# Kernel optimization log

Hardware: AMD Instinct MI355X
Metric: run time of the kernel (lower is better)

Reference implementation:

```python
import jax, jax.numpy as jnp
import numpy as np

# Fully-refined octree (branching=2, initial_levels=7) == dense grid of resolution 128.
R = 128            # voxel grid resolution per axis (2**initial_levels)
SH_DIM = 9         # (sh_degree+1)**2, sh_degree=2
DATA_DIM = 28      # 3*SH_DIM + 1 (RGB SH coeffs + density)
N_STEPS = 128      # fixed ray-march step count (render_opt.n_steps)
BG = 1.0           # background brightness


def sh_basis(d):
    """Real SH basis up to degree 2 for unit directions d: [N,3] -> [N,9]."""
    x, y, z = d[:, 0], d[:, 1], d[:, 2]
    C0 = 0.28209479177387814
    C1 = 0.4886025119029199
    C2 = (1.0925484305920792, -1.0925484305920792, 0.31539156525252005,
          -1.0925484305920792, 0.5462742152960396)
    return jnp.stack([
        jnp.full_like(x, C0),
        -C1 * y, C1 * z, -C1 * x,
        C2[0] * x * y, C2[1] * y * z,
        C2[2] * (2.0 * z * z - x * x - y * y),
        C2[3] * x * z, C2[4] * (x * x - y * y),
    ], axis=-1)


def trilerp(grid, pts):
    """Trilinear interpolation. grid [R,R,R,C], pts [N,3] in grid coords."""
    Rg = grid.shape[0]
    p = jnp.clip(pts, 0.0, Rg - 1.0 - 1e-4)
    p0 = jnp.floor(p).astype(jnp.int32)
    w = p - p0.astype(p.dtype)
    out = jnp.zeros((pts.shape[0], grid.shape[-1]), grid.dtype)
    for dx in (0, 1):
        wx = w[:, 0] if dx else 1.0 - w[:, 0]
        for dy in (0, 1):
            wy = w[:, 1] if dy else 1.0 - w[:, 1]
            for dz in (0, 1):
                wz = w[:, 2] if dz else 1.0 - w[:, 2]
                out = out + (wx * wy * wz)[:, None] * grid[p0[:, 0] + dx, p0[:, 1] + dy, p0[:, 2] + dz]
    return out


def _render(grid, rays_o, rays_d, scaling, offset):
    dirs = rays_d / jnp.linalg.norm(rays_d, axis=-1, keepdims=True)   # world viewdirs
    o = rays_o * scaling + offset                                      # tree coords in [0,1]^3
    d = dirs * scaling
    delta_scale = 1.0 / jnp.linalg.norm(d, axis=-1)                    # world-space step scale
    invd = 1.0 / jnp.where(jnp.abs(d) > 1e-9, d, 1e-9)
    t1 = (0.0 - o) * invd
    t2 = (1.0 - o) * invd
    tmin = jnp.maximum(jnp.max(jnp.minimum(t1, t2), axis=-1), 0.0)
    tmax = jnp.min(jnp.maximum(t1, t2), axis=-1)
    valid = tmax > tmin
    dt = jnp.where(valid, (tmax - tmin) / N_STEPS, 0.0)                # per-ray step length
    basis = sh_basis(dirs)                                             # [N,9]
    N = rays_o.shape[0]

    def step(carry, i):
        T, rgb = carry
        t = tmin + (i.astype(grid.dtype) + 0.5) * dt
        pos = o + t[:, None] * d                                       # [N,3] in [0,1]^3
        vals = trilerp(grid, pos * R - 0.5)                            # [N,28]
        sigma = jnp.where(valid, jax.nn.relu(vals[:, -1]), 0.0)
        coeffs = vals[:, :3 * SH_DIM].reshape(N, 3, SH_DIM)
        c = jax.nn.sigmoid(jnp.einsum('nj,ncj->nc', basis, coeffs))    # [N,3]
        alpha = 1.0 - jnp.exp(-sigma * dt * delta_scale)
        rgb = rgb + (T * alpha)[:, None] * c
        T = T * (1.0 - alpha)
        return (T, rgb), None

    init = (jnp.ones((N,), grid.dtype), jnp.zeros((N, 3), grid.dtype))
    (T, rgb), _ = jax.lax.scan(step, init, jnp.arange(N_STEPS))
    return rgb + T[:, None] * BG


def setup_inputs() -> dict:
    key = jax.random.key(0)
    k1, k2, k3 = jax.random.split(key, 3)
    N = 32768
    rays_o = jax.random.uniform(k1, (N, 3), jnp.float32)               # inside unit cube
    rays_d = jax.random.normal(k2, (N, 3), jnp.float32)
    grid = jax.random.normal(k3, (R, R, R, DATA_DIM), jnp.float32) * 0.1  # octree leaf data
    scaling = jnp.ones((3,), jnp.float32)                              # 0.5/radius, radius=0.5
    offset = jnp.zeros((3,), jnp.float32)                              # 0.5 - center*scaling
    return {"rays_o": rays_o, "rays_d": rays_d, "grid": grid,
            "scaling": scaling, "offset": offset}


def reference(rays_o, rays_d, grid, scaling, offset):
    return _render(grid, rays_o, rays_d, scaling, offset)
```

## Files before the change

kernel.cpp:

```cpp
#include <hip/hip_runtime.h>
#include <math.h>

#define RGRID 128
#define NSTEPS 128
#define DATA_DIM 28

__device__ __forceinline__ float fast_rcp(float x) { return __builtin_amdgcn_rcpf(x); }

__global__ __launch_bounds__(256) void render_kernel(
    const float* __restrict__ rays_o,
    const float* __restrict__ rays_d,
    const float* __restrict__ grid,
    const float* __restrict__ scaling,
    const float* __restrict__ offset,
    float* __restrict__ out, int N)
{
    int tid = blockIdx.x * blockDim.x + threadIdx.x;
    int ray = tid >> 6;
    int lane = tid & 63;
    int s = lane >> 3;
    int c = lane & 7;
    if (ray >= N) return;

    float ox = rays_o[ray * 3 + 0], oy = rays_o[ray * 3 + 1], oz = rays_o[ray * 3 + 2];
    float rdx = rays_d[ray * 3 + 0], rdy = rays_d[ray * 3 + 1], rdz = rays_d[ray * 3 + 2];
    float sx = scaling[0], sy = scaling[1], sz = scaling[2];
    float fx = offset[0], fy = offset[1], fz = offset[2];

    float dn = rsqrtf(rdx * rdx + rdy * rdy + rdz * rdz);
    float dirx = rdx * dn, diry = rdy * dn, dirz = rdz * dn;

    float o0 = ox * sx + fx, o1 = oy * sy + fy, o2 = oz * sz + fz;
    float d0 = dirx * sx, d1 = diry * sy, d2 = dirz * sz;
    float delta_scale = rsqrtf(d0 * d0 + d1 * d1 + d2 * d2);

    float a0 = fabsf(d0) > 1e-9f ? d0 : 1e-9f;
    float a1 = fabsf(d1) > 1e-9f ? d1 : 1e-9f;
    float a2 = fabsf(d2) > 1e-9f ? d2 : 1e-9f;
    float i0 = 1.0f / a0, i1 = 1.0f / a1, i2 = 1.0f / a2;

    float t1x = (0.0f - o0) * i0, t2x = (1.0f - o0) * i0;
    float t1y = (0.0f - o1) * i1, t2y = (1.0f - o1) * i1;
    float t1z = (0.0f - o2) * i2, t2z = (1.0f - o2) * i2;
    float tmin = fmaxf(fmaxf(fminf(t1x, t2x), fminf(t1y, t2y)), fminf(t1z, t2z));
    tmin = fmaxf(tmin, 0.0f);
    float tmax = fminf(fminf(fmaxf(t1x, t2x), fmaxf(t1y, t2y)), fmaxf(t1z, t2z));
    bool valid = tmax > tmin;
    float dt = valid ? (tmax - tmin) * (1.0f / NSTEPS) : 0.0f;
    float sig_scale = dt * delta_scale;

    const float C0 = 0.28209479177387814f;
    const float C1 = 0.4886025119029199f;
    float b0 = C0;
    float b1 = -C1 * diry;
    float b2 = C1 * dirz;
    float b3 = -C1 * dirx;
    float b4 = 1.0925484305920792f * dirx * diry;
    float b5 = -1.0925484305920792f * diry * dirz;
    float b6 = 0.31539156525252005f * (2.0f * dirz * dirz - dirx * dirx - diry * diry);
    float b7 = -1.0925484305920792f * dirx * dirz;
    float b8 = 0.5462742152960396f * (dirx * dirx - diry * diry);

    int cdx = (c >> 2) & 1, cdy = (c >> 1) & 1, cdz = c & 1;
    int laneoff = (cdx << 14) + (cdy << 7) + cdz;
    float fsx = cdx ? 1.0f : -1.0f, fbx = cdx ? 0.0f : 1.0f;
    float fsy = cdy ? 1.0f : -1.0f, fby = cdy ? 0.0f : 1.0f;
    float fsz = cdz ? 1.0f : -1.0f, fbz = cdz ? 0.0f : 1.0f;

    float T = 1.0f, accr = 0.0f, accg = 0.0f, accb = 0.0f;
    float soff = (float)s + 0.5f;

    auto calc = [&](int base, const float4*& gp, float& wgt) {
        float t = tmin + ((float)base + soff) * dt;
        float px = o0 + t * d0, py = o1 + t * d1, pz = o2 + t * d2;
        float gx = fminf(fmaxf(px * (float)RGRID - 0.5f, 0.0f), 126.9999f);
        float gy = fminf(fmaxf(py * (float)RGRID - 0.5f, 0.0f), 126.9999f);
        float gz = fminf(fmaxf(pz * (float)RGRID - 0.5f, 0.0f), 126.9999f);
        float flx = floorf(gx), fly = floorf(gy), flz = floorf(gz);
        int ix = (int)flx, iy = (int)fly, iz = (int)flz;
        float wx = gx - flx, wy = gy - fly, wz = gz - flz;
        wgt = (fsx * wx + fbx) * (fsy * wy + fby) * (fsz * wz + fbz);
        int vox = (ix << 14) + (iy << 7) + iz + laneoff;
        gp = (const float4*)(grid + (size_t)vox * DATA_DIM);
    };

    auto compute = [&](float4 v0, float4 v1, float4 v2, float4 v3,
                       float4 v4, float4 v5, float4 v6, float wgt) {
        float vr = b0 * v0.x + b1 * v0.y + b2 * v0.z + b3 * v0.w
                 + b4 * v1.x + b5 * v1.y + b6 * v1.z + b7 * v1.w + b8 * v2.x;
        float vg = b0 * v2.y + b1 * v2.z + b2 * v2.w
                 + b3 * v3.x + b4 * v3.y + b5 * v3.z + b6 * v3.w
                 + b7 * v4.x + b8 * v4.y;
        float vb = b0 * v4.z + b1 * v4.w
                 + b2 * v5.x + b3 * v5.y + b4 * v5.z + b5 * v5.w
                 + b6 * v6.x + b7 * v6.y + b8 * v6.z;
        float vs = v6.w;

        vr *= wgt; vg *= wgt; vb *= wgt; vs *= wgt;

        #pragma unroll
        for (int m = 1; m < 8; m <<= 1) {
            vr += __shfl_xor(vr, m);
            vg += __shfl_xor(vg, m);
            vb += __shfl_xor(vb, m);
            vs += __shfl_xor(vs, m);
        }

        float sigma = valid ? fmaxf(vs, 0.0f) : 0.0f;
        float alpha = 1.0f - __expf(-sigma * sig_scale);
        float av = 1.0f - alpha;
        float br = alpha * fast_rcp(1.0f + __expf(-vr));
        float bg = alpha * fast_rcp(1.0f + __expf(-vg));
        float bb = alpha * fast_rcp(1.0f + __expf(-vb));

        #pragma unroll
        for (int d = 8; d < 64; d <<= 1) {
            float pa  = __shfl_up(av, d);
            float pbr = __shfl_up(br, d);
            float pbg = __shfl_up(bg, d);
            float pbb = __shfl_up(bb, d);
            if (lane >= d) {
                br = pbr + pa * br;
                bg = pbg + pa * bg;
                bb = pbb + pa * bb;
                av = pa * av;
            }
        }

        accr += T * br;
        accg += T * bg;
        accb += T * bb;
        T *= av;
    };

    const float4 *gpA, *gpB;
    float wA, wB;
    float4 A0, A1, A2, A3, A4, A5, A6;
    float4 B0, B1, B2, B3, B4, B5, B6;

    calc(0, gpA, wA);
    A0 = gpA[0]; A1 = gpA[1]; A2 = gpA[2]; A3 = gpA[3];
    A4 = gpA[4]; A5 = gpA[5]; A6 = gpA[6];

    for (int base = 0; base < NSTEPS - 16; base += 16) {
        calc(base + 8, gpB, wB);
        B0 = gpB[0]; B1 = gpB[1]; B2 = gpB[2]; B3 = gpB[3];
        B4 = gpB[4]; B5 = gpB[5]; B6 = gpB[6];
        compute(A0, A1, A2, A3, A4, A5, A6, wA);

        calc(base + 16, gpA, wA);
        A0 = gpA[0]; A1 = gpA[1]; A2 = gpA[2]; A3 = gpA[3];
        A4 = gpA[4]; A5 = gpA[5]; A6 = gpA[6];
        compute(B0, B1, B2, B3, B4, B5, B6, wB);
    }

    calc(NSTEPS - 8, gpB, wB);
    B0 = gpB[0]; B1 = gpB[1]; B2 = gpB[2]; B3 = gpB[3];
    B4 = gpB[4]; B5 = gpB[5]; B6 = gpB[6];
    compute(A0, A1, A2, A3, A4, A5, A6, wA);
    compute(B0, B1, B2, B3, B4, B5, B6, wB);

    if (lane == 63) {
        out[ray * 3 + 0] = accr + T * 1.0f;
        out[ray * 3 + 1] = accg + T * 1.0f;
        out[ray * 3 + 2] = accb + T * 1.0f;
    }
}

extern "C" void kernel_launch(void* const* d_in, const int* in_sizes, int n_in,
                              void* d_out, int out_size, void* d_ws, size_t ws_size,
                              hipStream_t stream) {
    const float* rays_o  = (const float*)d_in[0];
    const float* rays_d  = (const float*)d_in[1];
    const float* grid    = (const float*)d_in[2];
    const float* scaling = (const float*)d_in[3];
    const float* offset  = (const float*)d_in[4];
    float* out = (float*)d_out;
    int N = in_sizes[0] / 3;

    int threads = 256;
    long long total = (long long)N * 64;
    int blocks = (int)((total + threads - 1) / threads);
    render_kernel<<<blocks, threads, 0, stream>>>(rays_o, rays_d, grid, scaling, offset, out, N);
}
```

Before: 502.7 us.

## Repack voxel grid to packed fp16 and use dot2 for SH evaluation

Each call first runs a pre-pass that converts the fp32 grid into 64-byte packed fp16 records, laid out so each colour's SH coefficients line up with the packed basis pairs. The render kernel then gathers half as many bytes per trilinear corner and evaluates the SH dot products with fdot2 instructions. This targets the gather bandwidth and cache footprint of the ray march. In exchange it adds a full-grid read and write on every call and lowers the precision of the stored coefficients and basis values. The fallback fp32 path, used when the workspace is too small, drops software pipelining and writes its result from lane 0 instead of lane 63, which looks wrong for the scanned transmittance.

```diff
diff --git a/kernel.cpp b/kernel.cpp
--- a/kernel.cpp
+++ b/kernel.cpp
@@ -4,10 +4,232 @@
 #define RGRID 128
 #define NSTEPS 128
 #define DATA_DIM 28
+#define NVOX (RGRID * RGRID * RGRID)
+
+typedef _Float16 h2 __attribute__((ext_vector_type(2)));
 
 __device__ __forceinline__ float fast_rcp(float x) { return __builtin_amdgcn_rcpf(x); }
 
-__global__ __launch_bounds__(256) void render_kernel(
+__device__ __forceinline__ float dot2acc(h2 a, h2 b, float c) {
+#if __has_builtin(__builtin_amdgcn_fdot2)
+    return __builtin_amdgcn_fdot2(a, b, c, false);
+#else
+    return c + (float)a[0] * (float)b[0] + (float)a[1] * (float)b[1];
+#endif
+}
+
+__device__ __forceinline__ unsigned pk(float a, float b) {
+    h2 t;
+    t[0] = (_Float16)a;
+    t[1] = (_Float16)b;
+    return __builtin_bit_cast(unsigned, t);
+}
+
+__device__ __forceinline__ h2 bc(unsigned w) { return __builtin_bit_cast(h2, w); }
+
+__global__ __launch_bounds__(256) void repack_kernel(
+    const float* __restrict__ grid, unsigned* __restrict__ ws)
+{
+    int v = blockIdx.x * blockDim.x + threadIdx.x;
+    if (v >= NVOX) return;
+    const float4* src = (const float4*)(grid + (size_t)v * DATA_DIM);
+    float4 f0 = src[0], f1 = src[1], f2 = src[2], f3 = src[3];
+    float4 f4 = src[4], f5 = src[5], f6 = src[6];
+
+    uint4 o0, o1, o2;
+    uint2 o3;
+    o0.x = pk(f0.x, f0.y); o0.y = pk(f0.z, f0.w); o0.z = pk(f1.x, f1.y); o0.w = pk(f1.z, f1.w);
+    o1.x = pk(f2.y, f2.z); o1.y = pk(f2.w, f3.x); o1.z = pk(f3.y, f3.z); o1.w = pk(f3.w, f4.x);
+    o2.x = pk(f4.z, f4.w); o2.y = pk(f5.x, f5.y); o2.z = pk(f5.z, f5.w); o2.w = pk(f6.x, f6.y);
+    o3.x = pk(f2.x, f4.y);
+    o3.y = pk(f6.z, f6.w);
+
+    unsigned* dst = ws + ((size_t)v << 4);
+    *(uint4*)(dst + 0) = o0;
+    *(uint4*)(dst + 4) = o1;
+    *(uint4*)(dst + 8) = o2;
+    *(uint2*)(dst + 12) = o3;
+}
+
+__global__ __launch_bounds__(256) void render_fp16(
+    const float* __restrict__ rays_o,
+    const float* __restrict__ rays_d,
+    const unsigned* __restrict__ vox16,
+    const float* __restrict__ scaling,
+    const float* __restrict__ offset,
+    float* __restrict__ out, int N)
+{
+    int tid = blockIdx.x * blockDim.x + threadIdx.x;
+    int ray = tid >> 6;
+    int lane = tid & 63;
+    int s = lane >> 3;
+    int c = lane & 7;
+    if (ray >= N) return;
+
+    float ox = rays_o[ray * 3 + 0], oy = rays_o[ray * 3 + 1], oz = rays_o[ray * 3 + 2];
+    float rdx = rays_d[ray * 3 + 0], rdy = rays_d[ray * 3 + 1], rdz = rays_d[ray * 3 + 2];
+    float sx = scaling[0], sy = scaling[1], sz = scaling[2];
+    float fx = offset[0], fy = offset[1], fz = offset[2];
+
+    float dn = rsqrtf(rdx * rdx + rdy * rdy + rdz * rdz);
+    float dirx = rdx * dn, diry = rdy * dn, dirz = rdz * dn;
+
+    float o0 = ox * sx + fx, o1 = oy * sy + fy, o2 = oz * sz + fz;
+    float d0 = dirx * sx, d1 = diry * sy, d2 = dirz * sz;
+    float delta_scale = rsqrtf(d0 * d0 + d1 * d1 + d2 * d2);
+
+    float a0 = fabsf(d0) > 1e-9f ? d0 : 1e-9f;
+    float a1 = fabsf(d1) > 1e-9f ? d1 : 1e-9f;
+    float a2 = fabsf(d2) > 1e-9f ? d2 : 1e-9f;
+    float i0 = 1.0f / a0, i1 = 1.0f / a1, i2 = 1.0f / a2;
+
+    float t1x = (0.0f - o0) * i0, t2x = (1.0f - o0) * i0;
+    float t1y = (0.0f - o1) * i1, t2y = (1.0f - o1) * i1;
+    float t1z = (0.0f - o2) * i2, t2z = (1.0f - o2) * i2;
+    float tmin = fmaxf(fmaxf(fminf(t1x, t2x), fminf(t1y, t2y)), fminf(t1z, t2z));
+    tmin = fmaxf(tmin, 0.0f);
+    float tmax = fminf(fminf(fmaxf(t1x, t2x), fmaxf(t1y, t2y)), fmaxf(t1z, t2z));
+    bool valid = tmax > tmin;
+    float dt = valid ? (tmax - tmin) * (1.0f / NSTEPS) : 0.0f;
+    float sig_scale = dt * delta_scale;
+
+    const float C0 = 0.28209479177387814f;
+    const float C1 = 0.4886025119029199f;
+    float b0f = C0;
+    float b1f = -C1 * diry;
+    float b2f = C1 * dirz;
+    float b3f = -C1 * dirx;
+    float b4f = 1.0925484305920792f * dirx * diry;
+    float b5f = -1.0925484305920792f * diry * dirz;
+    float b6f = 0.31539156525252005f * (2.0f * dirz * dirz - dirx * dirx - diry * diry);
+    float b7f = -1.0925484305920792f * dirx * dirz;
+    float b8f = 0.5462742152960396f * (dirx * dirx - diry * diry);
+    h2 hb01, hb23, hb45, hb67;
+    hb01[0] = (_Float16)b0f; hb01[1] = (_Float16)b1f;
+    hb23[0] = (_Float16)b2f; hb23[1] = (_Float16)b3f;
+    hb45[0] = (_Float16)b4f; hb45[1] = (_Float16)b5f;
+    hb67[0] = (_Float16)b6f; hb67[1] = (_Float16)b7f;
+
+    int cdx = (c >> 2) & 1, cdy = (c >> 1) & 1, cdz = c & 1;
+    int laneoff = (cdx << 14) + (cdy << 7) + cdz;
+    float fsx = cdx ? 1.0f : -1.0f, fbx = cdx ? 0.0f : 1.0f;
+    float fsy = cdy ? 1.0f : -1.0f, fby = cdy ? 0.0f : 1.0f;
+    float fsz = cdz ? 1.0f : -1.0f, fbz = cdz ? 0.0f : 1.0f;
+
+    float T = 1.0f, accr = 0.0f, accg = 0.0f, accb = 0.0f;
+    float soff = (float)s + 0.5f;
+
+    auto calc = [&](int base, const unsigned*& gp, float& wgt) {
+        float t = tmin + ((float)base + soff) * dt;
+        float px = o0 + t * d0, py = o1 + t * d1, pz = o2 + t * d2;
+        float gx = fminf(fmaxf(px * (float)RGRID - 0.5f, 0.0f), 126.9999f);
+        float gy = fminf(fmaxf(py * (float)RGRID - 0.5f, 0.0f), 126.9999f);
+        float gz = fminf(fmaxf(pz * (float)RGRID - 0.5f, 0.0f), 126.9999f);
+        float flx = floorf(gx), fly = floorf(gy), flz = floorf(gz);
+        int ix = (int)flx, iy = (int)fly, iz = (int)flz;
+        float wx = gx - flx, wy = gy - fly, wz = gz - flz;
+        wgt = (fsx * wx + fbx) * (fsy * wy + fby) * (fsz * wz + fbz);
+        int vox = (ix << 14) + (iy << 7) + iz + laneoff;
+        gp = vox16 + ((size_t)vox << 4);
+    };
+
+    auto compute = [&](uint4 A0, uint4 A1, uint4 A2, uint2 A3, float wgt) {
+        h2 e0 = bc(A3.x);
+        h2 e1 = bc(A3.y);
+        float vr = dot2acc(bc(A0.x), hb01,
+                   dot2acc(bc(A0.y), hb23,
+                   dot2acc(bc(A0.z), hb45,
+                   dot2acc(bc(A0.w), hb67, (float)e0[0] * b8f))));
+        float vg = dot2acc(bc(A1.x), hb01,
+                   dot2acc(bc(A1.y), hb23,
+                   dot2acc(bc(A1.z), hb45,
+                   dot2acc(bc(A1.w), hb67, (float)e0[1] * b8f))));
+        float vb = dot2acc(bc(A2.x), hb01,
+                   dot2acc(bc(A2.y), hb23,
+                   dot2acc(bc(A2.z), hb45,
+                   dot2acc(bc(A2.w), hb67, (float)e1[0] * b8f))));
+        float vs = (float)e1[1];
+
+        vr *= wgt; vg *= wgt; vb *= wgt; vs *= wgt;
+
+        #pragma unroll
+        for (int m = 1; m < 8; m <<= 1) {
+            vr += __shfl_xor(vr, m);
+            vg += __shfl_xor(vg, m);
+            vb += __shfl_xor(vb, m);
+            vs += __shfl_xor(vs, m);
+        }
+
+        float sigma = valid ? fmaxf(vs, 0.0f) : 0.0f;
+        float alpha = 1.0f - __expf(-sigma * sig_scale);
+        float av = 1.0f - alpha;
+        float br = alpha * fast_rcp(1.0f + __expf(-vr));
+        float bg = alpha * fast_rcp(1.0f + __expf(-vg));
+        float bb = alpha * fast_rcp(1.0f + __expf(-vb));
+
+        #pragma unroll
+        for (int d = 8; d < 64; d <<= 1) {
+            float pa  = __shfl_up(av, d);
+            float pbr = __shfl_up(br, d);
+            float pbg = __shfl_up(bg, d);
+            float pbb = __shfl_up(bb, d);
+            if (lane >= d) {
+                br = pbr + pa * br;
+                bg = pbg + pa * bg;
+                bb = pbb + pa * bb;
+                av = pa * av;
+            }
+        }
+
+        accr += T * br;
+        accg += T * bg;
+        accb += T * bb;
+        T *= av;
+    };
+
+    const unsigned *gpA, *gpB;
+    float wA, wB;
+    uint4 A0, A1, A2; uint2 A3;
+    uint4 B0, B1, B2; uint2 B3;
+
+    calc(0, gpA, wA);
+    A0 = *(const uint4*)(gpA + 0);
+    A1 = *(const uint4*)(gpA + 4);
+    A2 = *(const uint4*)(gpA + 8);
+    A3 = *(const uint2*)(gpA + 12);
+
+    for (int base = 0; base < NSTEPS - 16; base += 16) {
+        calc(base + 8, gpB, wB);
+        B0 = *(const uint4*)(gpB + 0);
+        B1 = *(const uint4*)(gpB + 4);
+        B2 = *(const uint4*)(gpB + 8);
+        B3 = *(const uint2*)(gpB + 12);
+        compute(A0, A1, A2, A3, wA);
+
+        calc(base + 16, gpA, wA);
+        A0 = *(const uint4*)(gpA + 0);
+        A1 = *(const uint4*)(gpA + 4);
+        A2 = *(const uint4*)(gpA + 8);
+        A3 = *(const uint2*)(gpA + 12);
+        compute(B0, B1, B2, B3, wB);
+    }
+
+    calc(NSTEPS - 8, gpB, wB);
+    B0 = *(const uint4*)(gpB + 0);
+    B1 = *(const uint4*)(gpB + 4);
+    B2 = *(const uint4*)(gpB + 8);
+    B3 = *(const uint2*)(gpB + 12);
+    compute(A0, A1, A2, A3, wA);
+    compute(B0, B1, B2, B3, wB);
+
+    if (lane == 63) {
+        out[ray * 3 + 0] = accr + T * 1.0f;
+        out[ray * 3 + 1] = accg + T * 1.0f;
+        out[ray * 3 + 2] = accb + T * 1.0f;
+    }
+}
+
+__global__ __launch_bounds__(256) void render_fp32(
     const float* __restrict__ rays_o,
     const float* __restrict__ rays_d,
     const float* __restrict__ grid,
@@ -70,22 +292,24 @@
     float T = 1.0f, accr = 0.0f, accg = 0.0f, accb = 0.0f;
     float soff = (float)s + 0.5f;
 
-    auto calc = [&](int base, const float4*& gp, float& wgt) {
-        float t = tmin + ((float)base + soff) * dt;
+    for (int it = 0; it < NSTEPS / 8; it++) {
+        float t = tmin + ((float)(it * 8) + soff) * dt;
         float px = o0 + t * d0, py = o1 + t * d1, pz = o2 + t * d2;
+
         float gx = fminf(fmaxf(px * (float)RGRID - 0.5f, 0.0f), 126.9999f);
         float gy = fminf(fmaxf(py * (float)RGRID - 0.5f, 0.0f), 126.9999f);
         float gz = fminf(fmaxf(pz * (float)RGRID - 0.5f, 0.0f), 126.9999f);
+
         float flx = floorf(gx), fly = floorf(gy), flz = floorf(gz);
         int ix = (int)flx, iy = (int)fly, iz = (int)flz;
         float wx = gx - flx, wy = gy - fly, wz = gz - flz;
-        wgt = (fsx * wx + fbx) * (fsy * wy + fby) * (fsz * wz + fbz);
+
+        float wgt = (fsx * wx + fbx) * (fsy * wy + fby) * (fsz * wz + fbz);
+
         int vox = (ix << 14) + (iy << 7) + iz + laneoff;
-        gp = (const float4*)(grid + (size_t)vox * DATA_DIM);
-    };
-
-    auto compute = [&](float4 v0, float4 v1, float4 v2, float4 v3,
-                       float4 v4, float4 v5, float4 v6, float wgt) {
+        const float4* gp = (const float4*)(grid + (size_t)vox * DATA_DIM);
+        float4 v0 = gp[0], v1 = gp[1], v2 = gp[2], v3 = gp[3], v4 = gp[4], v5 = gp[5], v6 = gp[6];
+
         float vr = b0 * v0.x + b1 * v0.y + b2 * v0.z + b3 * v0.w
                  + b4 * v1.x + b5 * v1.y + b6 * v1.z + b7 * v1.w + b8 * v2.x;
         float vg = b0 * v2.y + b1 * v2.z + b2 * v2.w
@@ -131,36 +355,9 @@
         accg += T * bg;
         accb += T * bb;
         T *= av;
-    };
-
-    const float4 *gpA, *gpB;
-    float wA, wB;
-    float4 A0, A1, A2, A3, A4, A5, A6;
-    float4 B0, B1, B2, B3, B4, B5, B6;
-
-    calc(0, gpA, wA);
-    A0 = gpA[0]; A1 = gpA[1]; A2 = gpA[2]; A3 = gpA[3];
-    A4 = gpA[4]; A5 = gpA[5]; A6 = gpA[6];
-
-    for (int base = 0; base < NSTEPS - 16; base += 16) {
-        calc(base + 8, gpB, wB);
-        B0 = gpB[0]; B1 = gpB[1]; B2 = gpB[2]; B3 = gpB[3];
-        B4 = gpB[4]; B5 = gpB[5]; B6 = gpB[6];
-        compute(A0, A1, A2, A3, A4, A5, A6, wA);
-
-        calc(base + 16, gpA, wA);
-        A0 = gpA[0]; A1 = gpA[1]; A2 = gpA[2]; A3 = gpA[3];
-        A4 = gpA[4]; A5 = gpA[5]; A6 = gpA[6];
-        compute(B0, B1, B2, B3, B4, B5, B6, wB);
-    }
-
-    calc(NSTEPS - 8, gpB, wB);
-    B0 = gpB[0]; B1 = gpB[1]; B2 = gpB[2]; B3 = gpB[3];
-    B4 = gpB[4]; B5 = gpB[5]; B6 = gpB[6];
-    compute(A0, A1, A2, A3, A4, A5, A6, wA);
-    compute(B0, B1, B2, B3, B4, B5, B6, wB);
-
-    if (lane == 63) {
+    }
+
+    if (lane == 0) {
         out[ray * 3 + 0] = accr + T * 1.0f;
         out[ray * 3 + 1] = accg + T * 1.0f;
         out[ray * 3 + 2] = accb + T * 1.0f;
@@ -181,5 +378,15 @@
     int threads = 256;
     long long total = (long long)N * 64;
     int blocks = (int)((total + threads - 1) / threads);
-    render_kernel<<<blocks, threads, 0, stream>>>(rays_o, rays_d, grid, scaling, offset, out, N);
-}
+
+    size_t need = (size_t)NVOX * 64;
+    if (ws_size >= need) {
+        int rblocks = (NVOX + threads - 1) / threads;
+        repack_kernel<<<rblocks, threads, 0, stream>>>(grid, (unsigned*)d_ws);
+        render_fp16<<<blocks, threads, 0, stream>>>(
+            rays_o, rays_d, (const unsigned*)d_ws, scaling, offset, out, N);
+    } else {
+        render_fp32<<<blocks, threads, 0, stream>>>(
+            rays_o, rays_d, grid, scaling, offset, out, N);
+    }
+}
```

New measurement: 502.1 us. About the same (-0.1%).
